# Kernel optimization log

Measured on AMD Instinct MI355X. Metric: run time of the kernel, lower is better.

## Reference

```python
import jax, jax.numpy as jnp
import numpy as np

PAST = 12
FUTURE = 12


def setup_inputs() -> dict:
    key = jax.random.key(0)
    k1, k2, k3, k4, k5 = jax.random.split(key, 5)
    B, L, D = 64, 256, 512
    inp = jax.random.normal(k1, (B, L, D), dtype=jnp.float32)
    W_t = jax.random.normal(k2, (FUTURE, PAST), dtype=jnp.float32) / np.sqrt(PAST)
    b_t = jax.random.normal(k3, (FUTURE,), dtype=jnp.float32) * 0.01
    W_s = jax.random.normal(k4, (D, D), dtype=jnp.float32) / np.sqrt(D)
    b_s = jax.random.normal(k5, (D,), dtype=jnp.float32) * 0.01
    return {"inp": inp, "W_t": W_t, "b_t": b_t, "W_s": W_s, "b_s": b_s}


def reference(inp, W_t, b_t, W_s, b_s):
    # inp: [B, L, D]. Sliding windows of size PAST -> W = L - PAST windows.
    B, L, D = inp.shape
    W = L - PAST
    # gather windows: [B, W, PAST, D]
    idx = jnp.arange(W)[:, None] + jnp.arange(PAST)[None, :]  # [W, PAST]
    x_win = inp[:, idx, :]  # [B, W, PAST, D]
    # temporal Linear(PAST -> FUTURE) along window-time axis
    t = jnp.einsum('bwpd,fp->bwfd', x_win, W_t) + b_t[None, None, :, None]
    # spatial Linear(D -> D) along last axis
    out = jnp.einsum('bwfd,ed->bwfe', t, W_s) + b_s
    return out  # [B, W, FUTURE, D]
```

## Files before the change

### kernel.cpp

```cpp
#include <hip/hip_runtime.h>

#define PAST 12
#define FUTURE 12
#define NB 64
#define NL 256
#define ND 512
#define NW 244

typedef unsigned short ushort_t;
typedef __attribute__((ext_vector_type(8))) short short8;
typedef __attribute__((ext_vector_type(4))) float floatx4;

__device__ inline unsigned int f2bf(float x) {
    unsigned int u = __float_as_uint(x);
    return (u + 0x7fffu + ((u >> 16) & 1u)) >> 16;
}

__global__ __launch_bounds__(256) void convert_inp(
    const float* __restrict__ in, ushort_t* __restrict__ out)
{
    const int i = (blockIdx.x * 256 + threadIdx.x) * 8;
    const float4 v0 = *(const float4*)(in + i);
    const float4 v1 = *(const float4*)(in + i + 4);
    uint4 o;
    o.x = f2bf(v0.x) | (f2bf(v0.y) << 16);
    o.y = f2bf(v0.z) | (f2bf(v0.w) << 16);
    o.z = f2bf(v1.x) | (f2bf(v1.y) << 16);
    o.w = f2bf(v1.z) | (f2bf(v1.w) << 16);
    *(uint4*)(out + i) = o;
}

__global__ __launch_bounds__(256) void prep_ws(
    const float* __restrict__ Ws, ushort_t* __restrict__ Wsb, float* __restrict__ S)
{
    const int row = blockIdx.x;
    const int t = threadIdx.x;
    const float2 v = *(const float2*)(Ws + (size_t)row * ND + t * 2);
    *(unsigned int*)(Wsb + (size_t)row * ND + t * 2) = f2bf(v.x) | (f2bf(v.y) << 16);
    float s = v.x + v.y;
#pragma unroll
    for (int o = 32; o > 0; o >>= 1) s += __shfl_down(s, o);
    __shared__ float red[4];
    if ((t & 63) == 0) red[t >> 6] = s;
    __syncthreads();
    if (t == 0) S[row] = red[0] + red[1] + red[2] + red[3];
}

#define BM 128
#define BN 128
#define BK 32

__global__ __launch_bounds__(256) void gemm_spatial(
    const ushort_t* __restrict__ A,
    const ushort_t* __restrict__ Bm,
    ushort_t* __restrict__ Y)
{
    __shared__ ushort_t As[BM * BK];
    __shared__ ushort_t Bs[BN * BK];

    const int tid  = threadIdx.x;
    const int wave = tid >> 6;
    const int lane = tid & 63;
    const int m0 = blockIdx.y * BM;
    const int n0 = blockIdx.x * BN;
    const int wm = (wave >> 1) * 64;
    const int wn = (wave & 1) * 64;

    floatx4 acc[4][4] = {};

    const int row_a = tid >> 2;
    const int ch_a  = (tid & 3) * 8;

    for (int k0 = 0; k0 < ND; k0 += BK) {
        __syncthreads();
#pragma unroll
        for (int r = 0; r < 2; ++r) {
            const ushort_t* ga = A + (size_t)(m0 + row_a + r * 64) * ND + k0 + ch_a;
            __builtin_amdgcn_global_load_lds(
                (const __attribute__((address_space(1))) unsigned int*)ga,
                (__attribute__((address_space(3))) unsigned int*)(As + (r * 256 + wave * 64) * 8),
                16, 0, 0);
        }
#pragma unroll
        for (int r = 0; r < 2; ++r) {
            const ushort_t* gb = Bm + (size_t)(n0 + row_a + r * 64) * ND + k0 + ch_a;
            __builtin_amdgcn_global_load_lds(
                (const __attribute__((address_space(1))) unsigned int*)gb,
                (__attribute__((address_space(3))) unsigned int*)(Bs + (r * 256 + wave * 64) * 8),
                16, 0, 0);
        }
        __syncthreads();

        const ushort_t* a_base = As + (wm + (lane & 15)) * BK + (lane >> 4) * 8;
        const ushort_t* b_base = Bs + (wn + (lane & 15)) * BK + (lane >> 4) * 8;
        short8 a[4], b[4];
#pragma unroll
        for (int t = 0; t < 4; ++t) {
            a[t] = *(const short8*)(a_base + t * 16 * BK);
            b[t] = *(const short8*)(b_base + t * 16 * BK);
        }
#pragma unroll
        for (int i = 0; i < 4; ++i)
#pragma unroll
            for (int j = 0; j < 4; ++j)
                acc[i][j] = __builtin_amdgcn_mfma_f32_16x16x32_bf16(a[i], b[j], acc[i][j], 0, 0, 0);
    }

#pragma unroll
    for (int i = 0; i < 4; ++i) {
        const int m_base = m0 + wm + i * 16 + (lane >> 4) * 4;
#pragma unroll
        for (int j = 0; j < 4; ++j) {
            const int n = n0 + wn + j * 16 + (lane & 15);
#pragma unroll
            for (int r = 0; r < 4; ++r) {
                Y[(size_t)(m_base + r) * ND + n] = (ushort_t)f2bf(acc[i][j][r]);
            }
        }
    }
}

#define WTILE 8

__global__ __launch_bounds__(256) void temporal_kernel(
    const ushort_t* __restrict__ Y,
    const float*    __restrict__ Wt,
    const float*    __restrict__ bt,
    const float*    __restrict__ bs,
    const float*    __restrict__ S,
    float*          __restrict__ Out)
{
    const int tid = threadIdx.x;
    const int b  = blockIdx.y;
    const int w0 = blockIdx.x * WTILE + (tid >> 7) * 4;
    const int eq = (tid & 127) * 4;

    const float4 Sv  = *(const float4*)(S + eq);
    const float4 bsv = *(const float4*)(bs + eq);

    float win[PAST + 3][4];
    const ushort_t* ybase = Y + ((size_t)(b * NL + w0)) * ND + eq;
#pragma unroll
    for (int i = 0; i < PAST + 3; ++i) {
        if (w0 + i < NL) {
            const uint2 v = *(const uint2*)(ybase + (size_t)i * ND);
            win[i][0] = __uint_as_float(v.x << 16);
            win[i][1] = __uint_as_float(v.x & 0xffff0000u);
            win[i][2] = __uint_as_float(v.y << 16);
            win[i][3] = __uint_as_float(v.y & 0xffff0000u);
        } else {
            win[i][0] = win[i][1] = win[i][2] = win[i][3] = 0.f;
        }
    }

#pragma unroll
    for (int w = 0; w < 4; ++w) {
        if (w0 + w < NW) {
            float* orow = Out + ((size_t)(b * NW + (w0 + w)) * FUTURE) * ND + eq;
#pragma unroll
            for (int f = 0; f < FUTURE; ++f) {
                const float btf = bt[f];
                float a0 = fmaf(btf, Sv.x, bsv.x);
                float a1 = fmaf(btf, Sv.y, bsv.y);
                float a2 = fmaf(btf, Sv.z, bsv.z);
                float a3 = fmaf(btf, Sv.w, bsv.w);
#pragma unroll
                for (int p = 0; p < PAST; ++p) {
                    const float c = Wt[f * PAST + p];
                    a0 = fmaf(c, win[w + p][0], a0);
                    a1 = fmaf(c, win[w + p][1], a1);
                    a2 = fmaf(c, win[w + p][2], a2);
                    a3 = fmaf(c, win[w + p][3], a3);
                }
                *(float4*)(orow + (size_t)f * ND) = make_float4(a0, a1, a2, a3);
            }
        }
    }
}

extern "C" void kernel_launch(void* const* d_in, const int* in_sizes, int n_in,
                              void* d_out, int out_size, void* d_ws, size_t ws_size,
                              hipStream_t stream) {
    const float* inp = (const float*)d_in[0];
    const float* Wt  = (const float*)d_in[1];
    const float* bt  = (const float*)d_in[2];
    const float* Ws  = (const float*)d_in[3];
    const float* bs  = (const float*)d_in[4];
    float* out = (float*)d_out;

    const size_t n_inp = (size_t)NB * NL * ND;
    ushort_t* Y     = (ushort_t*)d_ws;
    ushort_t* inp_b = (ushort_t*)((char*)d_ws + n_inp * 2);
    ushort_t* Ws_b  = (ushort_t*)((char*)d_ws + n_inp * 4);
    float*    S     = (float*)((char*)d_ws + n_inp * 4 + (size_t)ND * ND * 2);

    convert_inp<<<dim3(n_inp / 8 / 256), dim3(256), 0, stream>>>(inp, inp_b);
    prep_ws<<<dim3(ND), dim3(256), 0, stream>>>(Ws, Ws_b, S);
    gemm_spatial<<<dim3(ND / BN, (NB * NL) / BM), dim3(256), 0, stream>>>(inp_b, Ws_b, Y);
    temporal_kernel<<<dim3((NW + WTILE - 1) / WTILE, NB), dim3(256), 0, stream>>>(Y, Wt, bt, bs, S, out);
}
```

Before: 427.2 us.

## Swizzle block order for XCD locality, drop LDS in GEMM, nontemporal output stores

Remaps block indices in the convert, GEMM and temporal kernels so that consecutive blocks land in contiguous data regions per XCD (bid&7 striding), aiming to improve L2 locality on the multi-die MI355X. The GEMM is rewritten to 64x64 tiles that read MFMA operands directly from global memory with no LDS staging or barriers, relying on L2 and cache reuse. Output stores in the temporal kernel become nontemporal to avoid polluting caches with the large fp32 output. The risk is lower operand reuse per block and more global traffic in the GEMM.

```diff
diff --git a/kernel.cpp b/kernel.cpp
--- a/kernel.cpp
+++ b/kernel.cpp
@@ -19,7 +19,8 @@
 __global__ __launch_bounds__(256) void convert_inp(
     const float* __restrict__ in, ushort_t* __restrict__ out)
 {
-    const int i = (blockIdx.x * 256 + threadIdx.x) * 8;
+    const int swz = (blockIdx.x & 7) * 512 + (blockIdx.x >> 3);
+    const int i = (swz * 256 + threadIdx.x) * 8;
     const float4 v0 = *(const float4*)(in + i);
     const float4 v1 = *(const float4*)(in + i + 4);
     uint4 o;
@@ -46,71 +47,49 @@
     if (t == 0) S[row] = red[0] + red[1] + red[2] + red[3];
 }
 
-#define BM 128
-#define BN 128
-#define BK 32
+#define BM 64
+#define BN 64
 
 __global__ __launch_bounds__(256) void gemm_spatial(
     const ushort_t* __restrict__ A,
     const ushort_t* __restrict__ Bm,
     ushort_t* __restrict__ Y)
 {
-    __shared__ ushort_t As[BM * BK];
-    __shared__ ushort_t Bs[BN * BK];
-
     const int tid  = threadIdx.x;
     const int wave = tid >> 6;
     const int lane = tid & 63;
-    const int m0 = blockIdx.y * BM;
-    const int n0 = blockIdx.x * BN;
-    const int wm = (wave >> 1) * 64;
-    const int wn = (wave & 1) * 64;
 
-    floatx4 acc[4][4] = {};
+    const int bid = blockIdx.x;
+    const int idx = (bid & 7) * 256 + (bid >> 3);
+    const int n0 = (idx & 7) * BN;
+    const int m0 = (idx >> 3) * BM;
+    const int wm = (wave >> 1) * 32;
+    const int wn = (wave & 1) * 32;
 
-    const int row_a = tid >> 2;
-    const int ch_a  = (tid & 3) * 8;
+    const ushort_t* a0 = A  + (size_t)(m0 + wm + (lane & 15)) * ND + (lane >> 4) * 8;
+    const ushort_t* b0 = Bm + (size_t)(n0 + wn + (lane & 15)) * ND + (lane >> 4) * 8;
 
-    for (int k0 = 0; k0 < ND; k0 += BK) {
-        __syncthreads();
+    floatx4 acc[2][2] = {};
+
+#pragma unroll 4
+    for (int k0 = 0; k0 < ND; k0 += 32) {
+        short8 af[2], bq[2];
+        af[0] = *(const short8*)(a0 + k0);
+        af[1] = *(const short8*)(a0 + (size_t)16 * ND + k0);
+        bq[0] = *(const short8*)(b0 + k0);
+        bq[1] = *(const short8*)(b0 + (size_t)16 * ND + k0);
 #pragma unroll
-        for (int r = 0; r < 2; ++r) {
-            const ushort_t* ga = A + (size_t)(m0 + row_a + r * 64) * ND + k0 + ch_a;
-            __builtin_amdgcn_global_load_lds(
-                (const __attribute__((address_space(1))) unsigned int*)ga,
-                (__attribute__((address_space(3))) unsigned int*)(As + (r * 256 + wave * 64) * 8),
-                16, 0, 0);
-        }
+        for (int i = 0; i < 2; ++i)
 #pragma unroll
-        for (int r = 0; r < 2; ++r) {
-            const ushort_t* gb = Bm + (size_t)(n0 + row_a + r * 64) * ND + k0 + ch_a;
-            __builtin_amdgcn_global_load_lds(
-                (const __attribute__((address_space(1))) unsigned int*)gb,
-                (__attribute__((address_space(3))) unsigned int*)(Bs + (r * 256 + wave * 64) * 8),
-                16, 0, 0);
-        }
-        __syncthreads();
-
-        const ushort_t* a_base = As + (wm + (lane & 15)) * BK + (lane >> 4) * 8;
-        const ushort_t* b_base = Bs + (wn + (lane & 15)) * BK + (lane >> 4) * 8;
-        short8 a[4], b[4];
-#pragma unroll
-        for (int t = 0; t < 4; ++t) {
-            a[t] = *(const short8*)(a_base + t * 16 * BK);
-            b[t] = *(const short8*)(b_base + t * 16 * BK);
-        }
-#pragma unroll
-        for (int i = 0; i < 4; ++i)
-#pragma unroll
-            for (int j = 0; j < 4; ++j)
-                acc[i][j] = __builtin_amdgcn_mfma_f32_16x16x32_bf16(a[i], b[j], acc[i][j], 0, 0, 0);
+            for (int j = 0; j < 2; ++j)
+                acc[i][j] = __builtin_amdgcn_mfma_f32_16x16x32_bf16(af[i], bq[j], acc[i][j], 0, 0, 0);
     }
 
 #pragma unroll
-    for (int i = 0; i < 4; ++i) {
+    for (int i = 0; i < 2; ++i) {
         const int m_base = m0 + wm + i * 16 + (lane >> 4) * 4;
 #pragma unroll
-        for (int j = 0; j < 4; ++j) {
+        for (int j = 0; j < 2; ++j) {
             const int n = n0 + wn + j * 16 + (lane & 15);
 #pragma unroll
             for (int r = 0; r < 4; ++r) {
@@ -121,6 +100,7 @@
 }
 
 #define WTILE 8
+#define TGRID (((NW + WTILE - 1) / WTILE) * NB)
 
 __global__ __launch_bounds__(256) void temporal_kernel(
     const ushort_t* __restrict__ Y,
@@ -131,8 +111,11 @@
     float*          __restrict__ Out)
 {
     const int tid = threadIdx.x;
-    const int b  = blockIdx.y;
-    const int w0 = blockIdx.x * WTILE + (tid >> 7) * 4;
+    const int bid = blockIdx.x;
+    const int idx = (bid & 7) * (TGRID / 8) + (bid >> 3);
+    const int b   = idx / 31;
+    const int wx  = idx % 31;
+    const int w0 = wx * WTILE + (tid >> 7) * 4;
     const int eq = (tid & 127) * 4;
 
     const float4 Sv  = *(const float4*)(S + eq);
@@ -172,7 +155,9 @@
                     a2 = fmaf(c, win[w + p][2], a2);
                     a3 = fmaf(c, win[w + p][3], a3);
                 }
-                *(float4*)(orow + (size_t)f * ND) = make_float4(a0, a1, a2, a3);
+                floatx4 ov;
+                ov.x = a0; ov.y = a1; ov.z = a2; ov.w = a3;
+                __builtin_nontemporal_store(ov, (floatx4*)(orow + (size_t)f * ND));
             }
         }
     }
@@ -194,8 +179,8 @@
     ushort_t* Ws_b  = (ushort_t*)((char*)d_ws + n_inp * 4);
     float*    S     = (float*)((char*)d_ws + n_inp * 4 + (size_t)ND * ND * 2);
 
+    prep_ws<<<dim3(ND), dim3(256), 0, stream>>>(Ws, Ws_b, S);
     convert_inp<<<dim3(n_inp / 8 / 256), dim3(256), 0, stream>>>(inp, inp_b);
-    prep_ws<<<dim3(ND), dim3(256), 0, stream>>>(Ws, Ws_b, S);
-    gemm_spatial<<<dim3(ND / BN, (NB * NL) / BM), dim3(256), 0, stream>>>(inp_b, Ws_b, Y);
-    temporal_kernel<<<dim3((NW + WTILE - 1) / WTILE, NB), dim3(256), 0, stream>>>(Y, Wt, bt, bs, S, out);
+    gemm_spatial<<<dim3((NB * NL / BM) * (ND / BN)), dim3(256), 0, stream>>>(inp_b, Ws_b, Y);
+    temporal_kernel<<<dim3(TGRID), dim3(256), 0, stream>>>(Y, Wt, bt, bs, S, out);
 }
```

Result: slower. 475.8 us (+11.4%).
